# Performance work log

Hardware: AMD Instinct MI355X
Metric: run time of the kernel (lower is better)

## Reference

```python
import jax, jax.numpy as jnp
import numpy as np

V, E, H, D, C, L = 100000, 300, 512, 512, 20, 2048


def gru_cell(x, h, Wih, Whh, bih, bhh):
    # PyTorch GRUCell: gates packed as [r; z; n] along first axis of W (3H rows)
    gi = x @ Wih.T + bih  # [3H]
    gh = h @ Whh.T + bhh  # [3H]
    ir, iz, i_n = gi[:H], gi[H:2 * H], gi[2 * H:]
    hr, hz, h_n = gh[:H], gh[H:2 * H], gh[2 * H:]
    r = jax.nn.sigmoid(ir + hr)
    z = jax.nn.sigmoid(iz + hz)
    n = jnp.tanh(i_n + r * h_n)
    return (1.0 - z) * n + z * h


def setup_inputs() -> dict:
    key = jax.random.key(0)
    ks = jax.random.split(key, 15)
    g = lambda k, shape, sc: (jax.random.normal(k, shape, dtype=jnp.float32) * sc)
    return {
        "sequence": jax.random.randint(ks[0], (L,), 0, V),
        "emb": g(ks[1], (V, E), 0.1),
        "Wih_f": g(ks[2], (3 * H, E), 0.05),
        "Whh_f": g(ks[3], (3 * H, H), 0.05),
        "bih_f": g(ks[4], (3 * H,), 0.05),
        "bhh_f": g(ks[5], (3 * H,), 0.05),
        "Wih_b": g(ks[6], (3 * H, E), 0.05),
        "Whh_b": g(ks[7], (3 * H, H), 0.05),
        "bih_b": g(ks[8], (3 * H,), 0.05),
        "bhh_b": g(ks[9], (3 * H,), 0.05),
        "W1": g(ks[10], (D, 2 * H), 0.05),
        "b1": g(ks[11], (D,), 0.05),
        "W2": g(ks[12], (C, D), 0.05),
        "b2": g(ks[13], (C,), 0.05),
    }


def reference(sequence, emb, Wih_f, Whh_f, bih_f, bhh_f,
              Wih_b, Whh_b, bih_b, bhh_b, W1, b1, W2, b2):
    x = emb[sequence]  # [L, E] embedding lookup
    h0 = jnp.zeros((H,), dtype=emb.dtype)

    def step_f(h, xt):
        return gru_cell(xt, h, Wih_f, Whh_f, bih_f, bhh_f), None

    def step_b(h, xt):
        return gru_cell(xt, h, Wih_b, Whh_b, bih_b, bhh_b), None

    hf, _ = jax.lax.scan(step_f, h0, x)
    hb, _ = jax.lax.scan(step_b, h0, x[::-1])

    h = jnp.concatenate([hf, hb])[None, :]  # [1, 2H]
    hid = jax.nn.relu(h @ W1.T + b1)        # dropout is identity at eval
    logits = hid @ W2.T + b2                # [1, C]
    return jax.nn.softmax(logits, axis=-1)
```

## Files before the change

kernel.cpp:

```cpp
#include <hip/hip_runtime.h>
#include <math.h>

constexpr int SEQ_L = 2048;
constexpr int EDIM  = 300;
constexpr int NCLS  = 20;
constexpr unsigned SENT = 0xFFA5A5A5u;

typedef float f32x4 __attribute__((ext_vector_type(4)));

__global__ __launch_bounds__(256) void init_kernel(uint4* H) {
  const int NT = 513 * 256;
  int idx = blockIdx.x * blockDim.x + threadIdx.x;
  const uint4 z = {0u, 0u, 0u, 0u};
  const uint4 s = {SENT, SENT, SENT, SENT};
#pragma unroll
  for (int i = 0; i < 4; ++i) {
    int q = i * NT + idx;
    if (q < 524544) H[q] = (q < 256) ? z : s;
  }
}

__global__ __launch_bounds__(256) void gi_kernel(
    const int* __restrict__ seq, const float* __restrict__ emb,
    const float* __restrict__ Wih_f, const float* __restrict__ bih_f,
    const float* __restrict__ bhh_f,
    const float* __restrict__ Wih_b, const float* __restrict__ bih_b,
    const float* __restrict__ bhh_b,
    float* __restrict__ gi_f, float* __restrict__ gi_b) {
  const int d = blockIdx.y;
  const float* Wih = d ? Wih_b : Wih_f;
  const float* bih = d ? bih_b : bih_f;
  const float* bhh = d ? bhh_b : bhh_f;
  float* gi = d ? gi_b : gi_f;
  const int t0 = blockIdx.x * 8;
  const int tid = threadIdx.x;

  __shared__ float xs[8][304];

  for (int i = tid; i < 8 * 75; i += 256) {
    int tt = i / 75, u = i - tt * 75;
    int t = t0 + tt;
    int s = seq[d ? (SEQ_L - 1 - t) : t];
    const float4* p = reinterpret_cast<const float4*>(emb + (size_t)s * EDIM);
    float4 v = p[u];
    xs[tt][u * 4 + 0] = v.x; xs[tt][u * 4 + 1] = v.y;
    xs[tt][u * 4 + 2] = v.z; xs[tt][u * 4 + 3] = v.w;
  }
  __syncthreads();

  for (int rr = 0; rr < 6; ++rr) {
    int j = rr * 256 + tid;
    const float4* wrow = reinterpret_cast<const float4*>(Wih + (size_t)j * EDIM);
    float acc[8];
#pragma unroll
    for (int tt = 0; tt < 8; ++tt) acc[tt] = 0.0f;
    for (int q = 0; q < EDIM / 4; ++q) {
      float4 w = wrow[q];
#pragma unroll
      for (int tt = 0; tt < 8; ++tt)
        acc[tt] += w.x * xs[tt][4 * q] + w.y * xs[tt][4 * q + 1] +
                   w.z * xs[tt][4 * q + 2] + w.w * xs[tt][4 * q + 3];
    }
    float bb = bih[j] + (j < 1024 ? bhh[j] : 0.0f);
#pragma unroll
    for (int tt = 0; tt < 8; ++tt)
      gi[(size_t)(t0 + tt) * 1536 + j] = acc[tt] + bb;
  }
}

__global__ __launch_bounds__(512, 2) void rnn_kernel(
    const float* __restrict__ Whh_f, const float* __restrict__ bhh_f,
    const float* __restrict__ Whh_b, const float* __restrict__ bhh_b,
    const float* __restrict__ gi_f, const float* __restrict__ gi_b,
    float* Hbuf) {
  const int tid  = threadIdx.x;
  const int lane = tid & 63;
  const int w    = tid >> 6;
  const int blk  = blockIdx.x;
  const int dir  = blk >> 4;
  const int j0   = (blk & 15) * 32;

  const float* Whh = dir ? Whh_b : Whh_f;
  const float* bhh = dir ? bhh_b : bhh_f;
  const float* gi  = dir ? gi_b : gi_f;

  alignas(16) __shared__ float hsh[512];
  alignas(16) __shared__ float part[8][12][68];
  __shared__ float rsum[96];

  f32x4 Wv[24];
#pragma unroll
  for (int g = 0; g < 3; ++g)
#pragma unroll
    for (int jj = 0; jj < 4; ++jj) {
      const f32x4* rp = reinterpret_cast<const f32x4*>(
                            Whh + (size_t)(g * 512 + j0 + w * 4 + jj) * 512) +
                        lane * 2;
      Wv[(g * 4 + jj) * 2]     = rp[0];
      Wv[(g * 4 + jj) * 2 + 1] = rp[1];
    }

  const int jl = j0 + lane;
  float bhn = 0.0f;
  if (w == 0 && lane < 32) bhn = bhh[1024 + jl];
  float hprev = 0.0f;

  const int pollOff = dir * 512 + w * 64 + lane;

  for (int t = 0; t < SEQ_L; ++t) {
    float ir = 0.f, iz = 0.f, inn = 0.f;
    if (w == 0 && lane < 32) {
      const float* git = gi + (size_t)t * 1536;
      ir  = git[jl];
      iz  = git[512 + jl];
      inn = git[1024 + jl];
    }

    const float* hp = Hbuf + (size_t)t * 1024 + pollOff;
    float hvp;
    for (;;) {
      hvp = __hip_atomic_load(hp, __ATOMIC_RELAXED, __HIP_MEMORY_SCOPE_AGENT);
      if (__ballot(__float_as_uint(hvp) == SENT) == 0ull) break;
    }
    hsh[w * 64 + lane] = hvp;
    __syncthreads();

    const f32x4* hq = reinterpret_cast<const f32x4*>(&hsh[lane * 8]);
    f32x4 h0 = hq[0], h1 = hq[1];

    float s_[12];
#pragma unroll
    for (int r = 0; r < 12; ++r) {
      f32x4 w0 = Wv[2 * r], w1 = Wv[2 * r + 1];
      s_[r] = w0.x * h0.x + w0.y * h0.y + w0.z * h0.z + w0.w * h0.w +
              w1.x * h1.x + w1.y * h1.y + w1.z * h1.z + w1.w * h1.w;
    }

#pragma unroll
    for (int r = 0; r < 12; ++r) part[w][r][lane] = s_[r];
    __builtin_amdgcn_wave_barrier();
    if (lane < 12) {
      const f32x4* rowp = reinterpret_cast<const f32x4*>(&part[w][lane][0]);
      f32x4 a4 = rowp[0];
#pragma unroll
      for (int q = 1; q < 16; ++q) a4 += rowp[q];
      rsum[w * 12 + lane] = (a4.x + a4.y) + (a4.z + a4.w);
    }
    __syncthreads();

    if (w == 0 && lane < 32) {
      int ww = lane >> 2, jj = lane & 3;
      float sr = rsum[ww * 12 + jj];
      float sz = rsum[ww * 12 + 4 + jj];
      float sn = rsum[ww * 12 + 8 + jj];
      float rr = 1.0f / (1.0f + __expf(-(ir + sr)));
      float zz = 1.0f / (1.0f + __expf(-(iz + sz)));
      float nn = tanhf(inn + rr * (sn + bhn));
      float hnew = (1.0f - zz) * nn + zz * hprev;
      hprev = hnew;
      __hip_atomic_store(Hbuf + (size_t)(t + 1) * 1024 + dir * 512 + jl, hnew,
                         __ATOMIC_RELAXED, __HIP_MEMORY_SCOPE_AGENT);
    }
  }
}

__global__ __launch_bounds__(1024) void cls_kernel(
    const float* __restrict__ Hfin,
    const float* __restrict__ W1, const float* __restrict__ b1,
    const float* __restrict__ W2, const float* __restrict__ b2,
    float* __restrict__ out) {
  __shared__ float hcat[1024];
  __shared__ float hid[512];
  __shared__ float logits[NCLS];
  const int tid = threadIdx.x;
  hcat[tid] = Hfin[tid];
  __syncthreads();

  const int lane = tid & 63, widx = tid >> 6;
  for (int rr = 0; rr < 32; ++rr) {
    int row = widx * 32 + rr;
    const float4* wrow = reinterpret_cast<const float4*>(W1 + (size_t)row * 1024);
    float acc = 0.0f;
#pragma unroll
    for (int c = 0; c < 4; ++c) {
      int k = c * 256 + lane * 4;
      float4 v = wrow[c * 64 + lane];
      acc += v.x * hcat[k] + v.y * hcat[k + 1] + v.z * hcat[k + 2] +
             v.w * hcat[k + 3];
    }
#pragma unroll
    for (int mask = 32; mask >= 1; mask >>= 1) acc += __shfl_xor(acc, mask, 64);
    if (lane == 0) hid[row] = fmaxf(acc + b1[row], 0.0f);
  }
  __syncthreads();

  if (tid < NCLS) {
    const float4* wrow = reinterpret_cast<const float4*>(W2 + (size_t)tid * 512);
    float acc = 0.0f;
    for (int q = 0; q < 128; ++q) {
      float4 v = wrow[q];
      int k = q * 4;
      acc += v.x * hid[k] + v.y * hid[k + 1] + v.z * hid[k + 2] +
             v.w * hid[k + 3];
    }
    logits[tid] = acc + b2[tid];
  }
  __syncthreads();

  if (tid == 0) {
    float m = -1e30f;
    for (int i = 0; i < NCLS; ++i) m = fmaxf(m, logits[i]);
    float s = 0.0f;
    float e[NCLS];
    for (int i = 0; i < NCLS; ++i) { e[i] = __expf(logits[i] - m); s += e[i]; }
    float inv = 1.0f / s;
    for (int i = 0; i < NCLS; ++i) out[i] = e[i] * inv;
  }
}

extern "C" void kernel_launch(void* const* d_in, const int* in_sizes, int n_in,
                              void* d_out, int out_size, void* d_ws,
                              size_t ws_size, hipStream_t stream) {
  (void)in_sizes; (void)n_in; (void)out_size; (void)ws_size;
  const int*   seq   = (const int*)d_in[0];
  const float* emb   = (const float*)d_in[1];
  const float* Wih_f = (const float*)d_in[2];
  const float* Whh_f = (const float*)d_in[3];
  const float* bih_f = (const float*)d_in[4];
  const float* bhh_f = (const float*)d_in[5];
  const float* Wih_b = (const float*)d_in[6];
  const float* Whh_b = (const float*)d_in[7];
  const float* bih_b = (const float*)d_in[8];
  const float* bhh_b = (const float*)d_in[9];
  const float* W1    = (const float*)d_in[10];
  const float* b1    = (const float*)d_in[11];
  const float* W2    = (const float*)d_in[12];
  const float* b2    = (const float*)d_in[13];
  float* out = (float*)d_out;

  float* gi_f = (float*)d_ws;
  float* gi_b = gi_f + (size_t)SEQ_L * 1536;
  float* Hbuf = gi_b + (size_t)SEQ_L * 1536;

  hipLaunchKernelGGL(init_kernel, dim3(513), dim3(256), 0, stream,
                     (uint4*)Hbuf);
  hipLaunchKernelGGL(gi_kernel, dim3(SEQ_L / 8, 2), dim3(256), 0, stream,
                     seq, emb, Wih_f, bih_f, bhh_f, Wih_b, bih_b, bhh_b,
                     gi_f, gi_b);
  hipLaunchKernelGGL(rnn_kernel, dim3(32), dim3(512), 0, stream,
                     Whh_f, bhh_f, Whh_b, bhh_b, gi_f, gi_b, Hbuf);
  hipLaunchKernelGGL(cls_kernel, dim3(1), dim3(1024), 0, stream,
                     Hbuf + (size_t)SEQ_L * 1024, W1, b1, W2, b2, out);
}
```

Baseline: 4.085 ms.

## Place GRU recurrence workgroups on a shared XCD and poll via local cache

Launches 128 workgroups that report their XCC ID through a census buffer, then picks 16 per direction on the same XCD (or the two most populated XCDs) and lets the rest exit. Co-located groups poll the hidden-state buffer with sc0 loads, which can hit the shared L2, and fall back to agent-scope atomic polling after repeated misses. The per-step cross-wave __syncthreads for the gate reduction is replaced by per-wave shuffles, and h is double-buffered in shared memory. This targets the cross-XCD sync latency of the sequential recurrence. It adds a startup census and relies on the wait for all 128 blocks being co-resident and on the non-coherent loads eventually observing the stores.

```diff
diff --git a/kernel.cpp b/kernel.cpp
--- a/kernel.cpp
+++ b/kernel.cpp
@@ -5,6 +5,7 @@
 constexpr int EDIM  = 300;
 constexpr int NCLS  = 20;
 constexpr unsigned SENT = 0xFFA5A5A5u;
+constexpr int NWG = 128;
 
 typedef float f32x4 __attribute__((ext_vector_type(4)));
 
@@ -16,7 +17,7 @@
 #pragma unroll
   for (int i = 0; i < 4; ++i) {
     int q = i * NT + idx;
-    if (q < 524544) H[q] = (q < 256) ? z : s;
+    if (q < 524608) H[q] = (q < 256 || q >= 524544) ? z : s;
   }
 }
 
@@ -72,21 +73,76 @@
     const float* __restrict__ Whh_f, const float* __restrict__ bhh_f,
     const float* __restrict__ Whh_b, const float* __restrict__ bhh_b,
     const float* __restrict__ gi_f, const float* __restrict__ gi_b,
-    float* Hbuf) {
+    float* Hbuf, unsigned* census) {
   const int tid  = threadIdx.x;
   const int lane = tid & 63;
   const int w    = tid >> 6;
-  const int blk  = blockIdx.x;
-  const int dir  = blk >> 4;
-  const int j0   = (blk & 15) * 32;
+  const int bid  = blockIdx.x;
+
+  __shared__ int cen[NWG];
+  __shared__ int s_dir, s_slot, s_fast;
+
+  if (tid == 0) {
+    unsigned xcd;
+    asm volatile("s_getreg_b32 %0, hwreg(HW_REG_XCC_ID, 0, 32)" : "=s"(xcd));
+    __hip_atomic_store(&census[bid], (xcd & 7u) + 1u, __ATOMIC_RELAXED,
+                       __HIP_MEMORY_SCOPE_AGENT);
+  }
+  if (tid < NWG) {
+    unsigned v;
+    do {
+      v = __hip_atomic_load(&census[tid], __ATOMIC_RELAXED,
+                            __HIP_MEMORY_SCOPE_AGENT);
+    } while (v == 0u);
+    cen[tid] = (int)v - 1;
+  }
+  __syncthreads();
+
+  if (tid == 0) {
+    int counts[8] = {0, 0, 0, 0, 0, 0, 0, 0};
+    for (int i = 0; i < NWG; ++i) counts[cen[i]]++;
+    int x0 = 0;
+    for (int x = 1; x < 8; ++x) if (counts[x] > counts[x0]) x0 = x;
+    int x1, local1;
+    if (counts[x0] >= 32) { x1 = x0; local1 = 1; }
+    else {
+      int best = -1;
+      for (int x = 0; x < 8; ++x)
+        if (x != x0 && (best < 0 || counts[x] > counts[best])) best = x;
+      if (counts[best] >= 16) { x1 = best; local1 = 1; }
+      else { x1 = -1; local1 = 0; }
+    }
+    int myx = cen[bid];
+    int rankx = 0;
+    for (int i = 0; i < bid; ++i) if (cen[i] == myx) rankx++;
+    int dir = -1, slot = 0, fast = 0;
+    if (myx == x0 && rankx < 16) { dir = 0; slot = rankx; fast = 1; }
+    else if (local1 && x1 == x0 && myx == x0 && rankx >= 16 && rankx < 32) {
+      dir = 1; slot = rankx - 16; fast = 1;
+    } else if (local1 && x1 != x0 && myx == x1 && rankx < 16) {
+      dir = 1; slot = rankx; fast = 1;
+    } else if (!local1) {
+      int cx0 = 0, k = 0, rs = -1;
+      for (int i = 0; i < NWG; ++i) {
+        bool isd0 = (cen[i] == x0) && (cx0 < 16);
+        if (cen[i] == x0) cx0++;
+        if (!isd0) { if (i == bid) rs = k; k++; }
+      }
+      if (rs >= 0 && rs < 16) { dir = 1; slot = rs; fast = 0; }
+    }
+    s_dir = dir; s_slot = slot; s_fast = fast;
+  }
+  __syncthreads();
+  const int dir = s_dir, fast = s_fast;
+  if (dir < 0) return;
+  const int j0 = s_slot * 32;
 
   const float* Whh = dir ? Whh_b : Whh_f;
   const float* bhh = dir ? bhh_b : bhh_f;
   const float* gi  = dir ? gi_b : gi_f;
 
-  alignas(16) __shared__ float hsh[512];
+  alignas(16) __shared__ float hsh[2][512];
   alignas(16) __shared__ float part[8][12][68];
-  __shared__ float rsum[96];
 
   f32x4 Wv[24];
 #pragma unroll
@@ -100,32 +156,39 @@
       Wv[(g * 4 + jj) * 2 + 1] = rp[1];
     }
 
-  const int jl = j0 + lane;
   float bhn = 0.0f;
-  if (w == 0 && lane < 32) bhn = bhh[1024 + jl];
+  if (lane < 4) bhn = bhh[1024 + j0 + w * 4 + lane];
   float hprev = 0.0f;
-
-  const int pollOff = dir * 512 + w * 64 + lane;
+  int strikes = 0;
 
   for (int t = 0; t < SEQ_L; ++t) {
-    float ir = 0.f, iz = 0.f, inn = 0.f;
-    if (w == 0 && lane < 32) {
-      const float* git = gi + (size_t)t * 1536;
-      ir  = git[jl];
-      iz  = git[512 + jl];
-      inn = git[1024 + jl];
-    }
-
-    const float* hp = Hbuf + (size_t)t * 1024 + pollOff;
-    float hvp;
-    for (;;) {
-      hvp = __hip_atomic_load(hp, __ATOMIC_RELAXED, __HIP_MEMORY_SCOPE_AGENT);
-      if (__ballot(__float_as_uint(hvp) == SENT) == 0ull) break;
-    }
-    hsh[w * 64 + lane] = hvp;
+    float giv = 0.0f;
+    if (lane < 12)
+      giv = gi[(size_t)t * 1536 + (lane >> 2) * 512 + j0 + w * 4 + (lane & 3)];
+
+    const float* hp = Hbuf + (size_t)t * 1024 + dir * 512 + w * 64 + lane;
+    float hv = 0.0f;
+    bool got = false;
+    if (fast && strikes < 16) {
+      for (int it = 0; it < 64 && !got; ++it) {
+        unsigned u;
+        asm volatile("global_load_dword %0, %1, off sc0\n\ts_waitcnt vmcnt(0)"
+                     : "=v"(u) : "v"(hp) : "memory");
+        if (__ballot(u == SENT) == 0ull) { hv = __uint_as_float(u); got = true; }
+      }
+      if (!got) ++strikes;
+    }
+    if (!got) {
+      for (;;) {
+        float x = __hip_atomic_load(hp, __ATOMIC_RELAXED,
+                                    __HIP_MEMORY_SCOPE_AGENT);
+        if (__ballot(__float_as_uint(x) == SENT) == 0ull) { hv = x; break; }
+      }
+    }
+    hsh[t & 1][w * 64 + lane] = hv;
     __syncthreads();
 
-    const f32x4* hq = reinterpret_cast<const f32x4*>(&hsh[lane * 8]);
+    const f32x4* hq = reinterpret_cast<const f32x4*>(&hsh[t & 1][lane * 8]);
     f32x4 h0 = hq[0], h1 = hq[1];
 
     float s_[12];
@@ -139,27 +202,34 @@
 #pragma unroll
     for (int r = 0; r < 12; ++r) part[w][r][lane] = s_[r];
     __builtin_amdgcn_wave_barrier();
+    float red = 0.0f;
     if (lane < 12) {
       const f32x4* rowp = reinterpret_cast<const f32x4*>(&part[w][lane][0]);
       f32x4 a4 = rowp[0];
 #pragma unroll
       for (int q = 1; q < 16; ++q) a4 += rowp[q];
-      rsum[w * 12 + lane] = (a4.x + a4.y) + (a4.z + a4.w);
-    }
-    __syncthreads();
-
-    if (w == 0 && lane < 32) {
-      int ww = lane >> 2, jj = lane & 3;
-      float sr = rsum[ww * 12 + jj];
-      float sz = rsum[ww * 12 + 4 + jj];
-      float sn = rsum[ww * 12 + 8 + jj];
-      float rr = 1.0f / (1.0f + __expf(-(ir + sr)));
-      float zz = 1.0f / (1.0f + __expf(-(iz + sz)));
-      float nn = tanhf(inn + rr * (sn + bhn));
+      red = (a4.x + a4.y) + (a4.z + a4.w);
+    }
+    __builtin_amdgcn_wave_barrier();
+
+    float redf = red + ((lane < 8) ? giv : 0.0f);
+    int qq = lane & 3;
+    float v_r = __shfl(redf, qq, 64);
+    float v_z = __shfl(redf, 4 + qq, 64);
+    float v_n = __shfl(redf, 8 + qq, 64);
+    float v_i = __shfl(giv, 8 + qq, 64);
+    if (lane < 4) {
+      float rr = 1.0f / (1.0f + __expf(-v_r));
+      float zz = 1.0f / (1.0f + __expf(-v_z));
+      float nn = tanhf(v_i + rr * (v_n + bhn));
       float hnew = (1.0f - zz) * nn + zz * hprev;
       hprev = hnew;
-      __hip_atomic_store(Hbuf + (size_t)(t + 1) * 1024 + dir * 512 + jl, hnew,
-                         __ATOMIC_RELAXED, __HIP_MEMORY_SCOPE_AGENT);
+      float* dst = Hbuf + (size_t)(t + 1) * 1024 + dir * 512 + j0 + w * 4 + lane;
+      if (fast)
+        __hip_atomic_store(dst, hnew, __ATOMIC_RELAXED,
+                           __HIP_MEMORY_SCOPE_WORKGROUP);
+      __hip_atomic_store(dst, hnew, __ATOMIC_RELAXED,
+                         __HIP_MEMORY_SCOPE_AGENT);
     }
   }
 }
@@ -241,14 +311,15 @@
   float* gi_f = (float*)d_ws;
   float* gi_b = gi_f + (size_t)SEQ_L * 1536;
   float* Hbuf = gi_b + (size_t)SEQ_L * 1536;
+  unsigned* census = (unsigned*)(Hbuf + (size_t)2049 * 1024);
 
   hipLaunchKernelGGL(init_kernel, dim3(513), dim3(256), 0, stream,
                      (uint4*)Hbuf);
   hipLaunchKernelGGL(gi_kernel, dim3(SEQ_L / 8, 2), dim3(256), 0, stream,
                      seq, emb, Wih_f, bih_f, bhh_f, Wih_b, bih_b, bhh_b,
                      gi_f, gi_b);
-  hipLaunchKernelGGL(rnn_kernel, dim3(32), dim3(512), 0, stream,
-                     Whh_f, bhh_f, Whh_b, bhh_b, gi_f, gi_b, Hbuf);
+  hipLaunchKernelGGL(rnn_kernel, dim3(NWG), dim3(512), 0, stream,
+                     Whh_f, bhh_f, Whh_b, bhh_b, gi_f, gi_b, Hbuf, census);
   hipLaunchKernelGGL(cls_kernel, dim3(1), dim3(1024), 0, stream,
                      Hbuf + (size_t)SEQ_L * 1024, W1, b1, W2, b2, out);
 }
```

After: 7.325 ms. +79.3%, slower.

## Remove block barriers from GRU recurrence by per-wave polling and gate finalization

Applied to the files above, without the earlier changes.

Each wave now polls the full 512-wide hidden state it needs straight from global memory using 64-bit atomic loads, instead of one cooperative load into shared memory followed by __syncthreads. Each wave also finishes the gate math for its own 4 hidden units through wave-local shuffles, so the two block-wide barriers per timestep go away. This shortens the serial critical path of each step. The cost is 8x more polling traffic to L2 per block and gate work spread over 8 waves instead of one.

```diff
diff --git a/kernel.cpp b/kernel.cpp
--- a/kernel.cpp
+++ b/kernel.cpp
@@ -84,9 +84,7 @@
   const float* bhh = dir ? bhh_b : bhh_f;
   const float* gi  = dir ? gi_b : gi_f;
 
-  alignas(16) __shared__ float hsh[512];
   alignas(16) __shared__ float part[8][12][68];
-  __shared__ float rsum[96];
 
   f32x4 Wv[24];
 #pragma unroll
@@ -100,33 +98,39 @@
       Wv[(g * 4 + jj) * 2 + 1] = rp[1];
     }
 
-  const int jl = j0 + lane;
   float bhn = 0.0f;
-  if (w == 0 && lane < 32) bhn = bhh[1024 + jl];
+  if (lane < 4) bhn = bhh[1024 + j0 + w * 4 + lane];
   float hprev = 0.0f;
 
-  const int pollOff = dir * 512 + w * 64 + lane;
-
   for (int t = 0; t < SEQ_L; ++t) {
-    float ir = 0.f, iz = 0.f, inn = 0.f;
-    if (w == 0 && lane < 32) {
-      const float* git = gi + (size_t)t * 1536;
-      ir  = git[jl];
-      iz  = git[512 + jl];
-      inn = git[1024 + jl];
-    }
-
-    const float* hp = Hbuf + (size_t)t * 1024 + pollOff;
-    float hvp;
+    float giv = 0.0f;
+    if (lane < 12)
+      giv = gi[(size_t)t * 1536 + (lane >> 2) * 512 + j0 + w * 4 + (lane & 3)];
+
+    const unsigned long long* hp = reinterpret_cast<const unsigned long long*>(
+        Hbuf + (size_t)t * 1024 + dir * 512 + lane * 8);
+    unsigned long long p0, p1, p2, p3;
     for (;;) {
-      hvp = __hip_atomic_load(hp, __ATOMIC_RELAXED, __HIP_MEMORY_SCOPE_AGENT);
-      if (__ballot(__float_as_uint(hvp) == SENT) == 0ull) break;
-    }
-    hsh[w * 64 + lane] = hvp;
-    __syncthreads();
-
-    const f32x4* hq = reinterpret_cast<const f32x4*>(&hsh[lane * 8]);
-    f32x4 h0 = hq[0], h1 = hq[1];
+      p0 = __hip_atomic_load(hp + 0, __ATOMIC_RELAXED, __HIP_MEMORY_SCOPE_AGENT);
+      p1 = __hip_atomic_load(hp + 1, __ATOMIC_RELAXED, __HIP_MEMORY_SCOPE_AGENT);
+      p2 = __hip_atomic_load(hp + 2, __ATOMIC_RELAXED, __HIP_MEMORY_SCOPE_AGENT);
+      p3 = __hip_atomic_load(hp + 3, __ATOMIC_RELAXED, __HIP_MEMORY_SCOPE_AGENT);
+      unsigned bad =
+          ((unsigned)p0 == SENT) | ((unsigned)(p0 >> 32) == SENT) |
+          ((unsigned)p1 == SENT) | ((unsigned)(p1 >> 32) == SENT) |
+          ((unsigned)p2 == SENT) | ((unsigned)(p2 >> 32) == SENT) |
+          ((unsigned)p3 == SENT) | ((unsigned)(p3 >> 32) == SENT);
+      if (__ballot(bad != 0u) == 0ull) break;
+    }
+    f32x4 h0, h1;
+    h0.x = __uint_as_float((unsigned)p0);
+    h0.y = __uint_as_float((unsigned)(p0 >> 32));
+    h0.z = __uint_as_float((unsigned)p1);
+    h0.w = __uint_as_float((unsigned)(p1 >> 32));
+    h1.x = __uint_as_float((unsigned)p2);
+    h1.y = __uint_as_float((unsigned)(p2 >> 32));
+    h1.z = __uint_as_float((unsigned)p3);
+    h1.w = __uint_as_float((unsigned)(p3 >> 32));
 
     float s_[12];
 #pragma unroll
@@ -139,27 +143,31 @@
 #pragma unroll
     for (int r = 0; r < 12; ++r) part[w][r][lane] = s_[r];
     __builtin_amdgcn_wave_barrier();
+    float red = 0.0f;
     if (lane < 12) {
       const f32x4* rowp = reinterpret_cast<const f32x4*>(&part[w][lane][0]);
       f32x4 a4 = rowp[0];
 #pragma unroll
       for (int q = 1; q < 16; ++q) a4 += rowp[q];
-      rsum[w * 12 + lane] = (a4.x + a4.y) + (a4.z + a4.w);
-    }
-    __syncthreads();
-
-    if (w == 0 && lane < 32) {
-      int ww = lane >> 2, jj = lane & 3;
-      float sr = rsum[ww * 12 + jj];
-      float sz = rsum[ww * 12 + 4 + jj];
-      float sn = rsum[ww * 12 + 8 + jj];
-      float rr = 1.0f / (1.0f + __expf(-(ir + sr)));
-      float zz = 1.0f / (1.0f + __expf(-(iz + sz)));
-      float nn = tanhf(inn + rr * (sn + bhn));
+      red = (a4.x + a4.y) + (a4.z + a4.w);
+    }
+    __builtin_amdgcn_wave_barrier();
+
+    float redf = red + ((lane < 8) ? giv : 0.0f);
+    int qq = lane & 3;
+    float v_r = __shfl(redf, qq, 64);
+    float v_z = __shfl(redf, 4 + qq, 64);
+    float v_n = __shfl(redf, 8 + qq, 64);
+    float v_i = __shfl(giv, 8 + qq, 64);
+    if (lane < 4) {
+      float rr = 1.0f / (1.0f + __expf(-v_r));
+      float zz = 1.0f / (1.0f + __expf(-v_z));
+      float nn = tanhf(v_i + rr * (v_n + bhn));
       float hnew = (1.0f - zz) * nn + zz * hprev;
       hprev = hnew;
-      __hip_atomic_store(Hbuf + (size_t)(t + 1) * 1024 + dir * 512 + jl, hnew,
-                         __ATOMIC_RELAXED, __HIP_MEMORY_SCOPE_AGENT);
+      __hip_atomic_store(
+          Hbuf + (size_t)(t + 1) * 1024 + dir * 512 + j0 + w * 4 + lane, hnew,
+          __ATOMIC_RELAXED, __HIP_MEMORY_SCOPE_AGENT);
     }
   }
 }
```

Measured after the change: 8.851 ms. 2.17x slower.
